# Optimization experiments

Hardware: AMD Instinct MI355X
Metric: run time of the kernel (lower is better)

## Reference

```python
import jax, jax.numpy as jnp
import numpy as np

N_NODES = 100000


def _gcn_layer(x, src, dst, W, b, n):
    # PyG GCNConv: x' = x @ W, then symmetric-normalized aggregation with
    # self-loops (fill value 1), then + bias.
    h = x @ W  # [n, out]
    loop = jnp.arange(n, dtype=src.dtype)
    s = jnp.concatenate([src, loop])  # sources incl. self-loops
    d = jnp.concatenate([dst, loop])  # destinations incl. self-loops
    # degree computed on destination (col) with unit edge weights
    deg = jax.ops.segment_sum(jnp.ones_like(d, dtype=h.dtype), d, num_segments=n)
    dinv = jnp.where(deg > 0, jax.lax.rsqrt(deg), 0.0)
    norm = dinv[s] * dinv[d]  # [E+n]
    msg = h[s] * norm[:, None]  # gather + scale, [E+n, out]
    out = jax.ops.segment_sum(msg, d, num_segments=n)  # scatter-add
    return out + b


def setup_inputs() -> dict:
    key = jax.random.key(0)
    k1, k2, k3, k4, k5, k6 = jax.random.split(key, 6)
    in_c, hid_c, out_c = 5, 128, 64
    E = 1600000
    x = jax.random.normal(k1, (N_NODES, in_c), dtype=jnp.float32)
    edge_index = jax.random.randint(k2, (2, E), 0, N_NODES, dtype=jnp.int64)
    # Glorot-style init like PyG's Linear
    W1 = jax.random.normal(k3, (in_c, hid_c), dtype=jnp.float32) / np.sqrt(in_c)
    b1 = jnp.zeros((hid_c,), dtype=jnp.float32)
    W2 = jax.random.normal(k4, (hid_c, out_c), dtype=jnp.float32) / np.sqrt(hid_c)
    b2 = jnp.zeros((out_c,), dtype=jnp.float32)
    return {"x": x, "edge_index": edge_index, "W1": W1, "b1": b1, "W2": W2, "b2": b2}


def reference(x, edge_index, W1, b1, W2, b2):
    src, dst = edge_index[0], edge_index[1]
    n = x.shape[0]
    h = _gcn_layer(x, src, dst, W1, b1, n)
    h = jax.nn.relu(h)
    out = _gcn_layer(h, src, dst, W2, b2, n)
    return out
```

## Files before the change

### kernel.cpp

```cpp
#include <hip/hip_runtime.h>
#include <hip/hip_fp16.h>

#define IN_C 5
#define HID  128
#define OUTC 64

#define NBUCK_MAX 512
#define BCAP      4800
#define BIN_GRID  512
#define BIN_PER   3328
#define BIN_ITERS 13

typedef _Float16 f16x8 __attribute__((ext_vector_type(8)));
typedef float    f32x4 __attribute__((ext_vector_type(4)));

__global__ void __launch_bounds__(256)
k_init(const float* __restrict__ W2, __half* __restrict__ W2p,
       int* __restrict__ bucket_cnt) {
    if (blockIdx.x < 2) bucket_cnt[blockIdx.x * 256 + threadIdx.x] = 0;
    int i = blockIdx.x * 256 + threadIdx.x;
    int j = i & 7;
    int lane = (i >> 3) & 63;
    int kk = (i >> 9) & 3;
    int nt = i >> 11;
    int k = kk * 32 + (lane >> 4) * 8 + j;
    int nn = nt * 16 + (lane & 15);
    W2p[i] = __float2half(W2[k * OUTC + nn]);
}

__global__ void __launch_bounds__(256)
k_bin(const int* __restrict__ src, const int* __restrict__ dst,
      int* __restrict__ bucket_cnt, unsigned* __restrict__ binned, int E) {
    __shared__ int hist[NBUCK_MAX], base[NBUCK_MAX], lstart[NBUCK_MAX], cur[NBUCK_MAX];
    __shared__ unsigned staged[BIN_PER];
    __shared__ unsigned short sbuck[BIN_PER];
    int t = threadIdx.x;
    hist[t] = 0; hist[t + 256] = 0;
    __syncthreads();
    int per = (E + gridDim.x - 1) / gridDim.x;
    int lo = blockIdx.x * per, hi = min(E, lo + per);
    int ds[BIN_ITERS], ss[BIN_ITERS];
#pragma unroll
    for (int i = 0; i < BIN_ITERS; ++i) {
        int e = lo + t + i * 256;
        if (e < hi) {
            int d = dst[e];
            ds[i] = d; ss[i] = src[e];
            atomicAdd(&hist[d >> 8], 1);
        } else ds[i] = -1;
    }
    __syncthreads();
    if (hist[t] > 0)       base[t] = atomicAdd(&bucket_cnt[t], hist[t]);
    if (hist[t + 256] > 0) base[t + 256] = atomicAdd(&bucket_cnt[t + 256], hist[t + 256]);
    lstart[t] = hist[t]; lstart[t + 256] = hist[t + 256];
    __syncthreads();
#pragma unroll
    for (int off = 1; off < NBUCK_MAX; off <<= 1) {
        int a0 = (t >= off) ? lstart[t - off] : 0;
        int a1 = (t + 256 >= off) ? lstart[t + 256 - off] : 0;
        __syncthreads();
        lstart[t] += a0; lstart[t + 256] += a1;
        __syncthreads();
    }
    {
        int e0 = lstart[t] - hist[t];
        int e1 = lstart[t + 256] - hist[t + 256];
        __syncthreads();
        lstart[t] = e0; lstart[t + 256] = e1;
        cur[t] = e0; cur[t + 256] = e1;
    }
    __syncthreads();
#pragma unroll
    for (int i = 0; i < BIN_ITERS; ++i) {
        if (ds[i] >= 0) {
            int d = ds[i];
            int b = d >> 8;
            int pos = atomicAdd(&cur[b], 1);
            staged[pos] = ((unsigned)ss[i] << 8) | (unsigned)(d & 255);
            sbuck[pos] = (unsigned short)b;
        }
    }
    __syncthreads();
    int mtot = hi - lo;
    for (int s = t; s < mtot; s += 256) {
        int b = sbuck[s];
        binned[(size_t)b * BCAP + base[b] + (s - lstart[b])] = staged[s];
    }
}

__global__ void __launch_bounds__(256)
k_csr(const unsigned* __restrict__ binned, const int* __restrict__ bucket_cnt,
      const float* __restrict__ x,
      int* __restrict__ rowptr, int* __restrict__ cnt, float* __restrict__ dinv,
      __half* __restrict__ xs, int* __restrict__ col, int n, int nb) {
    __shared__ int sc[NBUCK_MAX];
    __shared__ int hist[256], sc2[256], cur[256];
    __shared__ int staged[BCAP];
    int b = blockIdx.x;
    int t = threadIdx.x;

    sc[t]       = (t < nb) ? bucket_cnt[t] : 0;
    sc[t + 256] = (t + 256 < nb) ? bucket_cnt[t + 256] : 0;
    __syncthreads();
#pragma unroll
    for (int off = 1; off < NBUCK_MAX; off <<= 1) {
        int a0 = (t >= off) ? sc[t - off] : 0;
        int a1 = (t + 256 >= off) ? sc[t + 256 - off] : 0;
        __syncthreads();
        sc[t] += a0; sc[t + 256] += a1;
        __syncthreads();
    }
    int m = bucket_cnt[b];
    int ebase = (b == 0) ? 0 : sc[b - 1];
    const unsigned* bin = binned + (size_t)b * BCAP;

    hist[t] = 0;
    __syncthreads();
    for (int e = t; e < m; e += 256)
        atomicAdd(&hist[bin[e] & 255], 1);
    __syncthreads();

    int h = hist[t];
    sc2[t] = h;
    __syncthreads();
#pragma unroll
    for (int off = 1; off < 256; off <<= 1) {
        int a = (t >= off) ? sc2[t - off] : 0;
        __syncthreads();
        sc2[t] += a;
        __syncthreads();
    }
    int rs = sc2[t] - h;
    cur[t] = rs;

    int v = b * 256 + t;
    if (v < n) {
        rowptr[v] = ebase + rs;
        cnt[v] = h;
        float dv = rsqrtf(1.0f + (float)h);
        dinv[v] = dv;
        const float* xp = x + (size_t)v * IN_C;
        __half2 hh[4];
        hh[0] = __floats2half2_rn(xp[0] * dv, xp[1] * dv);
        hh[1] = __floats2half2_rn(xp[2] * dv, xp[3] * dv);
        hh[2] = __floats2half2_rn(xp[4] * dv, 0.f);
        hh[3] = __floats2half2_rn(0.f, 0.f);
        *(uint4*)(xs + (size_t)v * 8) = *(uint4*)hh;
    }
    __syncthreads();
    for (int e = t; e < m; e += 256) {
        unsigned p = bin[e];
        int pos = atomicAdd(&cur[p & 255], 1);
        staged[pos] = (int)(p >> 8);
    }
    __syncthreads();
    for (int e = t; e < m; e += 256)
        col[ebase + e] = staged[e];
}

#define NB 64
#define H1STRIDE 132
__global__ void __launch_bounds__(256, 7)
k_fused(const __half* __restrict__ xs, const float* __restrict__ dinv,
        const int* __restrict__ rowptr, const int* __restrict__ cnt,
        const int* __restrict__ col,
        const float* __restrict__ W1, const float* __restrict__ b1,
        const __half* __restrict__ W2p, __half* __restrict__ g2, int n) {
    __shared__ __half sh_h1[NB * H1STRIDE];
    __shared__ float sh_xa[NB * 9];
    __shared__ float sh_dinv[NB];
    __shared__ int sh_start[NB], sh_len[NB];
    __shared__ __half2 sh_w1[IN_C * 64];
    __shared__ float sh_b1[HID];
    int t = threadIdx.x;
    int base = blockIdx.x * NB;

    for (int idx = t; idx < IN_C * 64; idx += 256) {
        int k = idx >> 6, jp = idx & 63;
        float2 w = *(const float2*)(W1 + k * HID + 2 * jp);
        sh_w1[idx] = __floats2half2_rn(w.x, w.y);
    }
    if (t < HID) sh_b1[t] = b1[t];

    if (t < NB) {
        int v = base + t;
        if (v < n) {
            sh_start[t] = rowptr[v];
            sh_len[t]   = cnt[v];
            sh_dinv[t]  = dinv[v];
        } else {
            sh_start[t] = 0; sh_len[t] = 0; sh_dinv[t] = 0.f;
        }
    }
    __syncthreads();

    {
        int q = t & 7;
#pragma unroll
        for (int half = 0; half < 2; ++half) {
            int vl = (t >> 3) + half * 32;
            int v = base + vl;
            int start = sh_start[vl], len = sh_len[vl];
            float a0 = 0.f, a1 = 0.f, a2 = 0.f, a3 = 0.f, a4 = 0.f;
            if (q == 0 && v < n) {
                uint4 r = *(const uint4*)(xs + (size_t)v * 8);
                const __half2* h = (const __half2*)&r;
                float2 f0 = __half22float2(h[0]), f1 = __half22float2(h[1]), f2 = __half22float2(h[2]);
                a0 = f0.x; a1 = f0.y; a2 = f1.x; a3 = f1.y; a4 = f2.x;
            }
            for (int k = q; k < len; k += 8) {
                int s = col[start + k];
                uint4 r = *(const uint4*)(xs + (size_t)s * 8);
                const __half2* h = (const __half2*)&r;
                float2 f0 = __half22float2(h[0]), f1 = __half22float2(h[1]), f2 = __half22float2(h[2]);
                a0 += f0.x; a1 += f0.y; a2 += f1.x; a3 += f1.y; a4 += f2.x;
            }
#pragma unroll
            for (int d = 1; d <= 4; d <<= 1) {
                a0 += __shfl_down(a0, d, 64);
                a1 += __shfl_down(a1, d, 64);
                a2 += __shfl_down(a2, d, 64);
                a3 += __shfl_down(a3, d, 64);
                a4 += __shfl_down(a4, d, 64);
            }
            if (q == 0) {
                float* sx = sh_xa + vl * 9;
                sx[0] = a0; sx[1] = a1; sx[2] = a2; sx[3] = a3; sx[4] = a4;
            }
        }
    }
    __syncthreads();

    {
        int v = t >> 2;
        const float* xa = sh_xa + v * 9;
        float x0 = xa[0], x1 = xa[1], x2 = xa[2], x3 = xa[3], x4 = xa[4];
        float dv = sh_dinv[v];
        __half* hrow = sh_h1 + v * H1STRIDE;
#pragma unroll
        for (int i = 0; i < 16; ++i) {
            int jp = (t & 3) + 4 * i;
            float2 w0 = __half22float2(sh_w1[jp]);
            float2 w1v = __half22float2(sh_w1[64 + jp]);
            float2 w2v = __half22float2(sh_w1[128 + jp]);
            float2 w3 = __half22float2(sh_w1[192 + jp]);
            float2 w4 = __half22float2(sh_w1[256 + jp]);
            float acc0 = x0 * w0.x + x1 * w1v.x + x2 * w2v.x + x3 * w3.x + x4 * w4.x;
            float acc1 = x0 * w0.y + x1 * w1v.y + x2 * w2v.y + x3 * w3.y + x4 * w4.y;
            int j0 = jp * 2;
            float2 bb = *(const float2*)(sh_b1 + j0);
            *(__half2*)(hrow + j0) =
                __floats2half2_rn(fmaxf(acc0 * dv + bb.x, 0.f), fmaxf(acc1 * dv + bb.y, 0.f));
        }
    }
    __syncthreads();

    {
        int w = t >> 6;
        int lane = t & 63;
        int quad = lane >> 4, nn = lane & 15;
        const __half* arow = sh_h1 + (size_t)(w * 16 + nn) * H1STRIDE + quad * 8;
        f16x8 afr[4];
#pragma unroll
        for (int kk = 0; kk < 4; ++kk)
            afr[kk] = *(const f16x8*)(arow + kk * 32);

        const f16x8* bp = (const f16x8*)W2p + lane;
#pragma unroll
        for (int nt = 0; nt < 4; ++nt) {
            f32x4 acc = {0.f, 0.f, 0.f, 0.f};
#pragma unroll
            for (int kk = 0; kk < 4; ++kk)
                acc = __builtin_amdgcn_mfma_f32_16x16x32_f16(
                    afr[kk], bp[(nt * 4 + kk) * 64], acc, 0, 0, 0);
#pragma unroll
            for (int r = 0; r < 4; ++r) {
                int vl = w * 16 + quad * 4 + r;
                int v = base + vl;
                if (v < n)
                    g2[(size_t)v * OUTC + nt * 16 + nn] =
                        __float2half(acc[r] * sh_dinv[vl]);
            }
        }
    }
}


#define MIX_LO(A, W) \
    asm("v_fma_mix_f32 %0, %1, %2, %0 op_sel:[0,0,0] op_sel_hi:[1,0,0]" \
        : "+v"(A) : "v"(W), "v"(one))
#define MIX_HI(A, W) \
    asm("v_fma_mix_f32 %0, %1, %2, %0 op_sel:[1,0,0] op_sel_hi:[1,0,0]" \
        : "+v"(A) : "v"(W), "v"(one))

#define ACC8(P, R)            \
    do {                      \
        MIX_LO(P##0, (R).x);  \
        MIX_HI(P##1, (R).x);  \
        MIX_LO(P##2, (R).y);  \
        MIX_HI(P##3, (R).y);  \
        MIX_LO(P##4, (R).z);  \
        MIX_HI(P##5, (R).z);  \
        MIX_LO(P##6, (R).w);  \
        MIX_HI(P##7, (R).w);  \
    } while (0)

__global__ void __launch_bounds__(256)
k_agg2(const __half* __restrict__ g2, const float* __restrict__ dinv,
       const int* __restrict__ rowptr, const int* __restrict__ cnt,
       const int* __restrict__ col, const float* __restrict__ b2,
       float* __restrict__ out, int n) {
    int t = threadIdx.x;
    int g = t >> 3;
    int oct = t & 7;
    int v = blockIdx.x * 32 + g;
    if (v >= n) return;

    int start = rowptr[v], len = cnt[v];
    float one = 1.0f;
    const __half* gb = g2 + (oct << 3);

    float a0 = 0.f, a1 = 0.f, a2 = 0.f, a3 = 0.f,
          a4 = 0.f, a5 = 0.f, a6 = 0.f, a7 = 0.f;
    float c0 = 0.f, c1 = 0.f, c2 = 0.f, c3 = 0.f,
          c4 = 0.f, c5 = 0.f, c6 = 0.f, c7 = 0.f;
    float e0 = 0.f, e1 = 0.f, e2 = 0.f, e3 = 0.f,
          e4 = 0.f, e5 = 0.f, e6 = 0.f, e7 = 0.f;
    float f0 = 0.f, f1 = 0.f, f2 = 0.f, f3 = 0.f,
          f4 = 0.f, f5 = 0.f, f6 = 0.f, f7 = 0.f;

    int it = 0;
    for (; it + 4 <= len; it += 4) {
        int s0 = col[start + it];
        int s1 = col[start + it + 1];
        int s2 = col[start + it + 2];
        int s3 = col[start + it + 3];
        uint4 r0 = *(const uint4*)(gb + ((size_t)s0 << 6));
        uint4 r1 = *(const uint4*)(gb + ((size_t)s1 << 6));
        uint4 r2 = *(const uint4*)(gb + ((size_t)s2 << 6));
        uint4 r3 = *(const uint4*)(gb + ((size_t)s3 << 6));
        ACC8(a, r0);
        ACC8(c, r1);
        ACC8(e, r2);
        ACC8(f, r3);
    }
    if (it + 2 <= len) {
        int s0 = col[start + it];
        int s1 = col[start + it + 1];
        uint4 r0 = *(const uint4*)(gb + ((size_t)s0 << 6));
        uint4 r1 = *(const uint4*)(gb + ((size_t)s1 << 6));
        ACC8(a, r0);
        ACC8(c, r1);
        it += 2;
    }
    if (it < len) {
        int s0 = col[start + it];
        uint4 r0 = *(const uint4*)(gb + ((size_t)s0 << 6));
        ACC8(e, r0);
    }

    {
        uint4 rs = *(const uint4*)(gb + ((size_t)v << 6));
        ACC8(f, rs);
    }

    a0 += c0; a1 += c1; a2 += c2; a3 += c3;
    a4 += c4; a5 += c5; a6 += c6; a7 += c7;
    e0 += f0; e1 += f1; e2 += f2; e3 += f3;
    e4 += f4; e5 += f5; e6 += f6; e7 += f7;
    a0 += e0; a1 += e1; a2 += e2; a3 += e3;
    a4 += e4; a5 += e5; a6 += e6; a7 += e7;

    float dv = dinv[v];
    const float* bp = b2 + (oct << 3);
    float4 bb0 = *(const float4*)bp;
    float4 bb1 = *(const float4*)(bp + 4);

    float4 o0 = make_float4(dv * a0 + bb0.x, dv * a1 + bb0.y,
                            dv * a2 + bb0.z, dv * a3 + bb0.w);
    float4 o1 = make_float4(dv * a4 + bb1.x, dv * a5 + bb1.y,
                            dv * a6 + bb1.z, dv * a7 + bb1.w);
    float4* op = (float4*)(out + ((size_t)v << 6) + (oct << 3));
    op[0] = o0;
    op[1] = o1;
}


extern "C" void kernel_launch(void* const* d_in, const int* in_sizes, int n_in,
                              void* d_out, int out_size, void* d_ws, size_t ws_size,
                              hipStream_t stream) {
    const float* x  = (const float*)d_in[0];
    const int*   ei = (const int*)d_in[1];
    const float* W1 = (const float*)d_in[2];
    const float* b1 = (const float*)d_in[3];
    const float* W2 = (const float*)d_in[4];
    const float* b2 = (const float*)d_in[5];
    float*       out = (float*)d_out;

    const int n = in_sizes[0] / IN_C;
    const int E = in_sizes[1] / 2;
    const int* src = ei;
    const int* dst = ei + E;
    const int nbuck = (n + 255) / 256;

    char* ws = (char*)d_ws;
    size_t off = 0;
    int* cnt         = (int*)(ws + off); off += (size_t)n * 4;
    int* rowptr      = (int*)(ws + off); off += (size_t)n * 4;
    int* col         = (int*)(ws + off); off += (size_t)E * 4;
    float* dinv      = (float*)(ws + off); off += (size_t)n * 4;
    __half* xs       = (__half*)(ws + off); off += (size_t)n * 8 * 2;
    __half* g2       = (__half*)(ws + off); off += (size_t)n * OUTC * 2;
    __half* W2p      = (__half*)(ws + off); off += (size_t)HID * OUTC * 2;
    int* bucket_cnt  = (int*)(ws + off); off += NBUCK_MAX * 4;
    unsigned* binned = (unsigned*)(ws + off); off += (size_t)NBUCK_MAX * BCAP * 4;

    const int B = 256;

    k_init<<<(HID * OUTC) / B, B, 0, stream>>>(W2, W2p, bucket_cnt);
    k_bin<<<BIN_GRID, B, 0, stream>>>(src, dst, bucket_cnt, binned, E);
    k_csr<<<nbuck, B, 0, stream>>>(binned, bucket_cnt, x,
                                   rowptr, cnt, dinv, xs, col, n, nbuck);

    k_fused<<<(n + NB - 1) / NB, B, 0, stream>>>(xs, dinv, rowptr, cnt, col,
                                                 W1, b1, W2p, g2, n);
    k_agg2<<<(n + 31) / 32, B, 0, stream>>>(g2, dinv, rowptr, cnt, col, b2, out, n);
}
```

Baseline: 169.0 us.

## Sort nodes by degree and remap block tiles for balanced aggregation

Adds a degree histogram, scan and permutation pass so the fused layer-1 kernel and the layer-2 aggregation visit nodes grouped by in-degree. Block indices are scrambled with a multiplicative stride, and the layer-2 kernel splits the 64 output channels into two 32-channel passes mapped to different XCD groups. The aim is to cut load imbalance between lanes and waves that share a node group, and to improve L2 locality per XCD. In exchange it adds three small kernel launches, an indirection through perm, and scattered output writes.

After: 217.4 us. +28.6%, slower.

```diff
diff --git a/kernel.cpp b/kernel.cpp
--- a/kernel.cpp
+++ b/kernel.cpp
@@ -16,8 +16,9 @@
 
 __global__ void __launch_bounds__(256)
 k_init(const float* __restrict__ W2, __half* __restrict__ W2p,
-       int* __restrict__ bucket_cnt) {
+       int* __restrict__ bucket_cnt, int* __restrict__ gdh) {
     if (blockIdx.x < 2) bucket_cnt[blockIdx.x * 256 + threadIdx.x] = 0;
+    if (blockIdx.x == 2) gdh[threadIdx.x] = 0;
     int i = blockIdx.x * 256 + threadIdx.x;
     int j = i & 7;
     int lane = (i >> 3) & 63;
@@ -158,22 +159,73 @@
         col[ebase + e] = staged[e];
 }
 
+
+__global__ void __launch_bounds__(256)
+k_dhist(const int* __restrict__ cnt, int* __restrict__ gdh, int n) {
+    __shared__ int h[256];
+    int t = threadIdx.x;
+    h[t] = 0;
+    __syncthreads();
+    int v = blockIdx.x * 256 + t;
+    if (v < n) atomicAdd(&h[min(cnt[v], 255)], 1);
+    __syncthreads();
+    if (h[t] > 0) atomicAdd(&gdh[t], h[t]);
+}
+
+__global__ void __launch_bounds__(256)
+k_dscan(int* __restrict__ gdh) {
+    __shared__ int s[256];
+    int t = threadIdx.x;
+    int h = gdh[t];
+    s[t] = h;
+    __syncthreads();
+#pragma unroll
+    for (int off = 1; off < 256; off <<= 1) {
+        int a = (t >= off) ? s[t - off] : 0;
+        __syncthreads();
+        s[t] += a;
+        __syncthreads();
+    }
+    gdh[t] = s[t] - h;
+}
+
+__global__ void __launch_bounds__(256)
+k_dperm(const int* __restrict__ cnt, int* __restrict__ gcur,
+        int* __restrict__ perm, int n) {
+    __shared__ int lh[256], lbase[256];
+    int t = threadIdx.x;
+    lh[t] = 0;
+    __syncthreads();
+    int v = blockIdx.x * 256 + t;
+    int bin = 0, lr = 0;
+    if (v < n) {
+        bin = min(cnt[v], 255);
+        lr = atomicAdd(&lh[bin], 1);
+    }
+    __syncthreads();
+    if (lh[t] > 0) lbase[t] = atomicAdd(&gcur[t], lh[t]);
+    __syncthreads();
+    if (v < n) perm[lbase[bin] + lr] = v;
+}
+
 #define NB 64
 #define H1STRIDE 132
 __global__ void __launch_bounds__(256, 7)
 k_fused(const __half* __restrict__ xs, const float* __restrict__ dinv,
         const int* __restrict__ rowptr, const int* __restrict__ cnt,
-        const int* __restrict__ col,
+        const int* __restrict__ col, const int* __restrict__ perm,
         const float* __restrict__ W1, const float* __restrict__ b1,
         const __half* __restrict__ W2p, __half* __restrict__ g2, int n) {
     __shared__ __half sh_h1[NB * H1STRIDE];
     __shared__ float sh_xa[NB * 9];
     __shared__ float sh_dinv[NB];
-    __shared__ int sh_start[NB], sh_len[NB];
+    __shared__ int sh_start[NB], sh_len[NB], sh_v[NB];
     __shared__ __half2 sh_w1[IN_C * 64];
     __shared__ float sh_b1[HID];
     int t = threadIdx.x;
-    int base = blockIdx.x * NB;
+    int nt_ = (n + NB - 1) / NB;
+    int tile = (int)(((long long)blockIdx.x * 97) % nt_);
+    int base = tile * NB;
 
     for (int idx = t; idx < IN_C * 64; idx += 256) {
         int k = idx >> 6, jp = idx & 63;
@@ -183,8 +235,10 @@
     if (t < HID) sh_b1[t] = b1[t];
 
     if (t < NB) {
-        int v = base + t;
-        if (v < n) {
+        int idx = base + t;
+        int v = (idx < n) ? perm[idx] : -1;
+        sh_v[t] = v;
+        if (v >= 0) {
             sh_start[t] = rowptr[v];
             sh_len[t]   = cnt[v];
             sh_dinv[t]  = dinv[v];
@@ -199,10 +253,10 @@
 #pragma unroll
         for (int half = 0; half < 2; ++half) {
             int vl = (t >> 3) + half * 32;
-            int v = base + vl;
+            int v = sh_v[vl];
             int start = sh_start[vl], len = sh_len[vl];
             float a0 = 0.f, a1 = 0.f, a2 = 0.f, a3 = 0.f, a4 = 0.f;
-            if (q == 0 && v < n) {
+            if (q == 0 && v >= 0) {
                 uint4 r = *(const uint4*)(xs + (size_t)v * 8);
                 const __half2* h = (const __half2*)&r;
                 float2 f0 = __half22float2(h[0]), f1 = __half22float2(h[1]), f2 = __half22float2(h[2]);
@@ -276,8 +330,8 @@
 #pragma unroll
             for (int r = 0; r < 4; ++r) {
                 int vl = w * 16 + quad * 4 + r;
-                int v = base + vl;
-                if (v < n)
+                int v = sh_v[vl];
+                if (v >= 0)
                     g2[(size_t)v * OUTC + nt * 16 + nn] =
                         __float2half(acc[r] * sh_dinv[vl]);
             }
@@ -308,17 +362,24 @@
 __global__ void __launch_bounds__(256)
 k_agg2(const __half* __restrict__ g2, const float* __restrict__ dinv,
        const int* __restrict__ rowptr, const int* __restrict__ cnt,
-       const int* __restrict__ col, const float* __restrict__ b2,
-       float* __restrict__ out, int n) {
-    int t = threadIdx.x;
-    int g = t >> 3;
-    int oct = t & 7;
-    int v = blockIdx.x * 32 + g;
-    if (v >= n) return;
+       const int* __restrict__ col, const int* __restrict__ perm,
+       const float* __restrict__ b2, float* __restrict__ out, int n) {
+    int t = threadIdx.x;
+    int b = blockIdx.x;
+    int xcd = b & 7;
+    int pass = xcd >> 2;
+    int NQ = (int)(gridDim.x >> 3);
+    int qmix = (int)(((long long)(b >> 3) * 97) % NQ);
+    int tile = qmix * 4 + (xcd & 3);
+    int g = t >> 2;
+    int oct = t & 3;
+    int idx = tile * 64 + g;
+    if (idx >= n) return;
+    int v = perm[idx];
 
     int start = rowptr[v], len = cnt[v];
     float one = 1.0f;
-    const __half* gb = g2 + (oct << 3);
+    const __half* gb = g2 + pass * 32 + (oct << 3);
 
     float a0 = 0.f, a1 = 0.f, a2 = 0.f, a3 = 0.f,
           a4 = 0.f, a5 = 0.f, a6 = 0.f, a7 = 0.f;
@@ -372,7 +433,7 @@
     a4 += e4; a5 += e5; a6 += e6; a7 += e7;
 
     float dv = dinv[v];
-    const float* bp = b2 + (oct << 3);
+    const float* bp = b2 + pass * 32 + (oct << 3);
     float4 bb0 = *(const float4*)bp;
     float4 bb1 = *(const float4*)(bp + 4);
 
@@ -380,7 +441,7 @@
                             dv * a2 + bb0.z, dv * a3 + bb0.w);
     float4 o1 = make_float4(dv * a4 + bb1.x, dv * a5 + bb1.y,
                             dv * a6 + bb1.z, dv * a7 + bb1.w);
-    float4* op = (float4*)(out + ((size_t)v << 6) + (oct << 3));
+    float4* op = (float4*)(out + ((size_t)v << 6) + pass * 32 + (oct << 3));
     op[0] = o0;
     op[1] = o1;
 }
@@ -409,20 +470,31 @@
     int* rowptr      = (int*)(ws + off); off += (size_t)n * 4;
     int* col         = (int*)(ws + off); off += (size_t)E * 4;
     float* dinv      = (float*)(ws + off); off += (size_t)n * 4;
+    int* perm        = (int*)(ws + off); off += (size_t)n * 4;
     __half* xs       = (__half*)(ws + off); off += (size_t)n * 8 * 2;
     __half* g2       = (__half*)(ws + off); off += (size_t)n * OUTC * 2;
     __half* W2p      = (__half*)(ws + off); off += (size_t)HID * OUTC * 2;
     int* bucket_cnt  = (int*)(ws + off); off += NBUCK_MAX * 4;
+    int* gdh         = (int*)(ws + off); off += 256 * 4;
     unsigned* binned = (unsigned*)(ws + off); off += (size_t)NBUCK_MAX * BCAP * 4;
 
     const int B = 256;
 
-    k_init<<<(HID * OUTC) / B, B, 0, stream>>>(W2, W2p, bucket_cnt);
+    k_init<<<(HID * OUTC) / B, B, 0, stream>>>(W2, W2p, bucket_cnt, gdh);
     k_bin<<<BIN_GRID, B, 0, stream>>>(src, dst, bucket_cnt, binned, E);
     k_csr<<<nbuck, B, 0, stream>>>(binned, bucket_cnt, x,
                                    rowptr, cnt, dinv, xs, col, n, nbuck);
 
-    k_fused<<<(n + NB - 1) / NB, B, 0, stream>>>(xs, dinv, rowptr, cnt, col,
+    k_dhist<<<nbuck, B, 0, stream>>>(cnt, gdh, n);
+    k_dscan<<<1, B, 0, stream>>>(gdh);
+    k_dperm<<<nbuck, B, 0, stream>>>(cnt, gdh, perm, n);
+
+    k_fused<<<(n + NB - 1) / NB, B, 0, stream>>>(xs, dinv, rowptr, cnt, col, perm,
                                                  W1, b1, W2p, g2, n);
-    k_agg2<<<(n + 31) / 32, B, 0, stream>>>(g2, dinv, rowptr, cnt, col, b2, out, n);
-}
+    {
+        int nt_ = (n + 63) / 64;
+        int nq  = (nt_ + 3) / 4;
+        k_agg2<<<nq * 8, B, 0, stream>>>(g2, dinv, rowptr, cnt, col, perm,
+                                         b2, out, n);
+    }
+}
```

## Split g2 into column-quarter planes and pin each quarter to XCD pairs

Applied to the files above, without the earlier changes.

The layer-1 output g2 is now written as four planes of 16 fp16 columns each, one plane per 16-column slice, instead of row-major 64-wide rows. The aggregation kernel maps block IDs so each pair of XCDs handles one quarter plane, with 2 threads per node and 128 nodes per block. Each XCD's L2 then caches only a quarter of g2, about 3.2MB, which should raise gather hit rates on the random neighbour reads. The cost is that each node's neighbour list and col indices are read four times, once per quarter, and the row-pointer and dinv loads are repeated as well.

After: 190.1 us. 1.12x slower.

```diff
diff --git a/kernel.cpp b/kernel.cpp
--- a/kernel.cpp
+++ b/kernel.cpp
@@ -266,6 +266,7 @@
             afr[kk] = *(const f16x8*)(arow + kk * 32);
 
         const f16x8* bp = (const f16x8*)W2p + lane;
+        size_t qstride = (size_t)n * 16;
 #pragma unroll
         for (int nt = 0; nt < 4; ++nt) {
             f32x4 acc = {0.f, 0.f, 0.f, 0.f};
@@ -278,7 +279,7 @@
                 int vl = w * 16 + quad * 4 + r;
                 int v = base + vl;
                 if (v < n)
-                    g2[(size_t)v * OUTC + nt * 16 + nn] =
+                    g2[(size_t)nt * qstride + (size_t)v * 16 + nn] =
                         __float2half(acc[r] * sh_dinv[vl]);
             }
         }
@@ -311,14 +312,18 @@
        const int* __restrict__ col, const float* __restrict__ b2,
        float* __restrict__ out, int n) {
     int t = threadIdx.x;
-    int g = t >> 3;
-    int oct = t & 7;
-    int v = blockIdx.x * 32 + g;
+    int b = blockIdx.x;
+    int xcd = b & 7;
+    int q = xcd >> 1;
+    int tile = (b >> 3) * 2 + (xcd & 1);
+    int g = t >> 1;
+    int o = t & 1;
+    int v = tile * 128 + g;
     if (v >= n) return;
 
     int start = rowptr[v], len = cnt[v];
     float one = 1.0f;
-    const __half* gb = g2 + (oct << 3);
+    const __half* gq = g2 + (size_t)q * ((size_t)n * 16) + (o << 3);
 
     float a0 = 0.f, a1 = 0.f, a2 = 0.f, a3 = 0.f,
           a4 = 0.f, a5 = 0.f, a6 = 0.f, a7 = 0.f;
@@ -335,10 +340,10 @@
         int s1 = col[start + it + 1];
         int s2 = col[start + it + 2];
         int s3 = col[start + it + 3];
-        uint4 r0 = *(const uint4*)(gb + ((size_t)s0 << 6));
-        uint4 r1 = *(const uint4*)(gb + ((size_t)s1 << 6));
-        uint4 r2 = *(const uint4*)(gb + ((size_t)s2 << 6));
-        uint4 r3 = *(const uint4*)(gb + ((size_t)s3 << 6));
+        uint4 r0 = *(const uint4*)(gq + ((size_t)s0 << 4));
+        uint4 r1 = *(const uint4*)(gq + ((size_t)s1 << 4));
+        uint4 r2 = *(const uint4*)(gq + ((size_t)s2 << 4));
+        uint4 r3 = *(const uint4*)(gq + ((size_t)s3 << 4));
         ACC8(a, r0);
         ACC8(c, r1);
         ACC8(e, r2);
@@ -347,20 +352,20 @@
     if (it + 2 <= len) {
         int s0 = col[start + it];
         int s1 = col[start + it + 1];
-        uint4 r0 = *(const uint4*)(gb + ((size_t)s0 << 6));
-        uint4 r1 = *(const uint4*)(gb + ((size_t)s1 << 6));
+        uint4 r0 = *(const uint4*)(gq + ((size_t)s0 << 4));
+        uint4 r1 = *(const uint4*)(gq + ((size_t)s1 << 4));
         ACC8(a, r0);
         ACC8(c, r1);
         it += 2;
     }
     if (it < len) {
         int s0 = col[start + it];
-        uint4 r0 = *(const uint4*)(gb + ((size_t)s0 << 6));
+        uint4 r0 = *(const uint4*)(gq + ((size_t)s0 << 4));
         ACC8(e, r0);
     }
 
     {
-        uint4 rs = *(const uint4*)(gb + ((size_t)v << 6));
+        uint4 rs = *(const uint4*)(gq + ((size_t)v << 4));
         ACC8(f, rs);
     }
 
@@ -372,7 +377,7 @@
     a4 += e4; a5 += e5; a6 += e6; a7 += e7;
 
     float dv = dinv[v];
-    const float* bp = b2 + (oct << 3);
+    const float* bp = b2 + q * 16 + (o << 3);
     float4 bb0 = *(const float4*)bp;
     float4 bb1 = *(const float4*)(bp + 4);
 
@@ -380,7 +385,7 @@
                             dv * a2 + bb0.z, dv * a3 + bb0.w);
     float4 o1 = make_float4(dv * a4 + bb1.x, dv * a5 + bb1.y,
                             dv * a6 + bb1.z, dv * a7 + bb1.w);
-    float4* op = (float4*)(out + ((size_t)v << 6) + (oct << 3));
+    float4* op = (float4*)(out + ((size_t)v << 6) + q * 16 + (o << 3));
     op[0] = o0;
     op[1] = o1;
 }
@@ -424,5 +429,10 @@
 
     k_fused<<<(n + NB - 1) / NB, B, 0, stream>>>(xs, dinv, rowptr, cnt, col,
                                                  W1, b1, W2p, g2, n);
-    k_agg2<<<(n + 31) / 32, B, 0, stream>>>(g2, dinv, rowptr, cnt, col, b2, out, n);
-}
+    {
+        int ntile = (n + 127) / 128;
+        int npair = (ntile + 1) / 2;
+        k_agg2<<<npair * 8, B, 0, stream>>>(g2, dinv, rowptr, cnt, col,
+                                            b2, out, n);
+    }
+}
```

## Split g2 into column halves and stage CSR columns in LDS for aggregation

Applied to the files above, without the earlier changes.

The layer-2 features g2 are now stored as two planar halves of 32 columns each instead of one 64-wide row. The aggregation kernel now handles 64 nodes per block with 4 threads per node, and processes the two halves one after the other. Each block first copies its contiguous slice of the CSR column indices into shared memory, so the neighbor-index reads come from LDS rather than global memory. This is meant to cut repeated index traffic and shrink the gathered footprint per pass. The cost is that each neighbor index is read twice, gathers are 64-byte segments, and nothing checks that a block's edges fit the fixed 2048-entry shared buffer.

Result: slower. 176.2 us (+4.2%).

```diff
diff --git a/kernel.cpp b/kernel.cpp
--- a/kernel.cpp
+++ b/kernel.cpp
@@ -10,6 +10,9 @@
 #define BIN_GRID  512
 #define BIN_PER   3328
 #define BIN_ITERS 13
+
+#define AGG_NB     64
+#define SH_COL_CAP 2048
 
 typedef _Float16 f16x8 __attribute__((ext_vector_type(8)));
 typedef float    f32x4 __attribute__((ext_vector_type(4)));
@@ -266,6 +269,7 @@
             afr[kk] = *(const f16x8*)(arow + kk * 32);
 
         const f16x8* bp = (const f16x8*)W2p + lane;
+        size_t hstride = (size_t)n * 32;
 #pragma unroll
         for (int nt = 0; nt < 4; ++nt) {
             f32x4 acc = {0.f, 0.f, 0.f, 0.f};
@@ -278,7 +282,7 @@
                 int vl = w * 16 + quad * 4 + r;
                 int v = base + vl;
                 if (v < n)
-                    g2[(size_t)v * OUTC + nt * 16 + nn] =
+                    g2[(size_t)(nt >> 1) * hstride + (size_t)v * 32 + (nt & 1) * 16 + nn] =
                         __float2half(acc[r] * sh_dinv[vl]);
             }
         }
@@ -305,21 +309,12 @@
         MIX_HI(P##7, (R).w);  \
     } while (0)
 
-__global__ void __launch_bounds__(256)
-k_agg2(const __half* __restrict__ g2, const float* __restrict__ dinv,
-       const int* __restrict__ rowptr, const int* __restrict__ cnt,
-       const int* __restrict__ col, const float* __restrict__ b2,
-       float* __restrict__ out, int n) {
-    int t = threadIdx.x;
-    int g = t >> 3;
-    int oct = t & 7;
-    int v = blockIdx.x * 32 + g;
-    if (v >= n) return;
-
-    int start = rowptr[v], len = cnt[v];
+__device__ __forceinline__ void agg_half(const __half* __restrict__ gq,
+                                         const int* __restrict__ sh_col,
+                                         int off, int len, int v, float dv,
+                                         const float* __restrict__ b2h,
+                                         float* __restrict__ outp) {
     float one = 1.0f;
-    const __half* gb = g2 + (oct << 3);
-
     float a0 = 0.f, a1 = 0.f, a2 = 0.f, a3 = 0.f,
           a4 = 0.f, a5 = 0.f, a6 = 0.f, a7 = 0.f;
     float c0 = 0.f, c1 = 0.f, c2 = 0.f, c3 = 0.f,
@@ -331,36 +326,35 @@
 
     int it = 0;
     for (; it + 4 <= len; it += 4) {
-        int s0 = col[start + it];
-        int s1 = col[start + it + 1];
-        int s2 = col[start + it + 2];
-        int s3 = col[start + it + 3];
-        uint4 r0 = *(const uint4*)(gb + ((size_t)s0 << 6));
-        uint4 r1 = *(const uint4*)(gb + ((size_t)s1 << 6));
-        uint4 r2 = *(const uint4*)(gb + ((size_t)s2 << 6));
-        uint4 r3 = *(const uint4*)(gb + ((size_t)s3 << 6));
+        int s0 = sh_col[off + it];
+        int s1 = sh_col[off + it + 1];
+        int s2 = sh_col[off + it + 2];
+        int s3 = sh_col[off + it + 3];
+        uint4 r0 = *(const uint4*)(gq + ((size_t)s0 << 5));
+        uint4 r1 = *(const uint4*)(gq + ((size_t)s1 << 5));
+        uint4 r2 = *(const uint4*)(gq + ((size_t)s2 << 5));
+        uint4 r3 = *(const uint4*)(gq + ((size_t)s3 << 5));
         ACC8(a, r0);
         ACC8(c, r1);
         ACC8(e, r2);
         ACC8(f, r3);
     }
     if (it + 2 <= len) {
-        int s0 = col[start + it];
-        int s1 = col[start + it + 1];
-        uint4 r0 = *(const uint4*)(gb + ((size_t)s0 << 6));
-        uint4 r1 = *(const uint4*)(gb + ((size_t)s1 << 6));
+        int s0 = sh_col[off + it];
+        int s1 = sh_col[off + it + 1];
+        uint4 r0 = *(const uint4*)(gq + ((size_t)s0 << 5));
+        uint4 r1 = *(const uint4*)(gq + ((size_t)s1 << 5));
         ACC8(a, r0);
         ACC8(c, r1);
         it += 2;
     }
     if (it < len) {
-        int s0 = col[start + it];
-        uint4 r0 = *(const uint4*)(gb + ((size_t)s0 << 6));
+        int s0 = sh_col[off + it];
+        uint4 r0 = *(const uint4*)(gq + ((size_t)s0 << 5));
         ACC8(e, r0);
     }
-
     {
-        uint4 rs = *(const uint4*)(gb + ((size_t)v << 6));
+        uint4 rs = *(const uint4*)(gq + ((size_t)v << 5));
         ACC8(f, rs);
     }
 
@@ -371,18 +365,50 @@
     a0 += e0; a1 += e1; a2 += e2; a3 += e3;
     a4 += e4; a5 += e5; a6 += e6; a7 += e7;
 
-    float dv = dinv[v];
-    const float* bp = b2 + (oct << 3);
-    float4 bb0 = *(const float4*)bp;
-    float4 bb1 = *(const float4*)(bp + 4);
-
+    float4 bb0 = *(const float4*)b2h;
+    float4 bb1 = *(const float4*)(b2h + 4);
     float4 o0 = make_float4(dv * a0 + bb0.x, dv * a1 + bb0.y,
                             dv * a2 + bb0.z, dv * a3 + bb0.w);
     float4 o1 = make_float4(dv * a4 + bb1.x, dv * a5 + bb1.y,
                             dv * a6 + bb1.z, dv * a7 + bb1.w);
-    float4* op = (float4*)(out + ((size_t)v << 6) + (oct << 3));
+    float4* op = (float4*)outp;
     op[0] = o0;
     op[1] = o1;
+}
+
+__global__ void __launch_bounds__(256)
+k_agg2(const __half* __restrict__ g2, const float* __restrict__ dinv,
+       const int* __restrict__ rowptr, const int* __restrict__ cnt,
+       const int* __restrict__ col, const float* __restrict__ b2,
+       float* __restrict__ out, int n) {
+    __shared__ int sh_col[SH_COL_CAP];
+    int t = threadIdx.x;
+    int base = blockIdx.x * AGG_NB;
+    int g = t >> 2;
+    int o = t & 2 ? 2 : (t & 3);
+    o = t & 3;
+    int v = base + g;
+
+    int start0 = rowptr[base];
+    int lastv = min(n - 1, base + AGG_NB - 1);
+    int m = rowptr[lastv] + cnt[lastv] - start0;
+    for (int e = t; e < m; e += 256)
+        sh_col[e] = col[start0 + e];
+    __syncthreads();
+
+    if (v >= n) return;
+    int off = rowptr[v] - start0;
+    int len = cnt[v];
+    float dv = dinv[v];
+
+    size_t hstride = (size_t)n * 32;
+    const __half* g2a = g2 + (o << 3);
+    const __half* g2b = g2 + hstride + (o << 3);
+
+    agg_half(g2a, sh_col, off, len, v, dv,
+             b2 + (o << 3), out + ((size_t)v << 6) + (o << 3));
+    agg_half(g2b, sh_col, off, len, v, dv,
+             b2 + 32 + (o << 3), out + ((size_t)v << 6) + 32 + (o << 3));
 }
 
 
@@ -424,5 +450,6 @@
 
     k_fused<<<(n + NB - 1) / NB, B, 0, stream>>>(xs, dinv, rowptr, cnt, col,
                                                  W1, b1, W2p, g2, n);
-    k_agg2<<<(n + 31) / 32, B, 0, stream>>>(g2, dinv, rowptr, cnt, col, b2, out, n);
-}
+    k_agg2<<<(n + AGG_NB - 1) / AGG_NB, B, 0, stream>>>(g2, dinv, rowptr, cnt,
+                                                        col, b2, out, n);
+}
```
